# Kernel optimization log

Measured on AMD Instinct MI355X. Metric: run time of the kernel, lower is better.

## Reference

```python
import jax, jax.numpy as jnp
import numpy as np

M, K, N, G = 4096, 4096, 4096, 128


def setup_inputs() -> dict:
    key = jax.random.key(0)
    k1, k2, k3 = jax.random.split(key, 3)
    a = jax.random.normal(k1, (M, K), dtype=jnp.float16)
    # 4-bit unsigned quantized weights, values in [0, 16)
    w_q = jax.random.randint(k2, (K, N), 0, 16, dtype=jnp.int32)
    # group-wise scales: one per (k-group, n); small magnitude keeps fp16 output in range
    scale = jax.random.uniform(k3, (K // G, N), dtype=jnp.float16, minval=0.001, maxval=0.02)
    return {"a": a, "w_q": w_q, "scale": scale, "group_size": G}


def reference(a, w_q, scale, group_size):
    # Dequantize: w[k, n] = w_q[k, n] * scale[k // group_size, n]
    scale_full = jnp.repeat(scale, group_size, axis=0)  # [K, N]
    w = w_q.astype(a.dtype) * scale_full                # fp16 dequantized weight
    out = jnp.matmul(a, w, preferred_element_type=jnp.float32)
    return out.astype(jnp.float16)
```

## Files before the change

### kernel.cpp

```cpp
#include <hip/hip_runtime.h>
#include <hip/hip_fp16.h>

#define MDIM 4096
#define NDIM 4096
#define KDIM 4096

#define BM 128
#define BN 128
#define BK 64
#define NT 256

typedef _Float16 f16x8 __attribute__((ext_vector_type(8)));
typedef float f32x4 __attribute__((ext_vector_type(4)));
typedef unsigned int u32;
typedef unsigned short u16;

__device__ inline __half2 as_half2(u32 u) { return __builtin_bit_cast(__half2, u); }
__device__ inline u32 as_u32(__half2 h) { return __builtin_bit_cast(u32, h); }
__device__ inline u32 pkrtz(float a, float b) {
  return __builtin_bit_cast(u32, __builtin_amdgcn_cvt_pkrtz(a, b));
}

__device__ inline void load16_to_lds(const void* g, void* l) {
  __builtin_amdgcn_global_load_lds(
      (__attribute__((address_space(1))) const u32*)g,
      (__attribute__((address_space(3))) u32*)l,
      16, 0, 0);
}

__global__ __launch_bounds__(NT) void a_to_f16(const float* __restrict__ A,
                                               _Float16* __restrict__ A16) {
  const size_t base = ((size_t)blockIdx.x * NT + threadIdx.x) * 8;
  const float4 f0 = *(const float4*)(A + base);
  const float4 f1 = *(const float4*)(A + base + 4);
  u32 pk[4];
  pk[0] = pkrtz(f0.x, f0.y);
  pk[1] = pkrtz(f0.z, f0.w);
  pk[2] = pkrtz(f1.x, f1.y);
  pk[3] = pkrtz(f1.z, f1.w);
  *(uint4*)(A16 + base) = *(const uint4*)pk;
}

#define TSTR 68
__global__ __launch_bounds__(NT) void w_dequant_t(const int* __restrict__ Wq,
                                                  const float* __restrict__ Sc,
                                                  _Float16* __restrict__ Wt) {
  __shared__ __align__(16) u16 Ls[64 * TSTR];
  const int tid = threadIdx.x;
  const int n0 = (blockIdx.x & 63) * 64;
  const int k0 = (blockIdx.x >> 6) * 64;
  const int g = k0 >> 7;

#pragma unroll
  for (int r = 0; r < 4; ++r) {
    const int c = r * 256 + tid;
    const int krow = c >> 4;
    const int col4 = (c & 15) * 4;
    const int4 v = *(const int4*)(Wq + (size_t)(k0 + krow) * NDIM + n0 + col4);
    const float4 s = *(const float4*)(Sc + (size_t)g * NDIM + n0 + col4);
    __half2 s01 = __floats2half2_rn(s.x, s.y);
    __half2 s23 = __floats2half2_rn(s.z, s.w);
    const __half2 kneg = __half2half2(__float2half(-1024.0f));
    __half2 nb01 = __hmul2(s01, kneg), nb23 = __hmul2(s23, kneg);
    u32 u01 = (u32)v.x | ((u32)v.y << 16) | 0x64006400u;
    u32 u23 = (u32)v.z | ((u32)v.w << 16) | 0x64006400u;
    u32 pk[2];
    pk[0] = as_u32(__hfma2(as_half2(u01), s01, nb01));
    pk[1] = as_u32(__hfma2(as_half2(u23), s23, nb23));
    *(uint2*)&Ls[(size_t)krow * TSTR + col4] = *(const uint2*)pk;
  }
  __syncthreads();

#pragma unroll
  for (int r = 0; r < 2; ++r) {
    const int idx = r * 256 + tid;
    const int n = idx >> 3;
    const int kc = (idx & 7) * 8;
    u16 tmp[8];
#pragma unroll
    for (int j = 0; j < 8; ++j) tmp[j] = Ls[(size_t)(kc + j) * TSTR + n];
    *(uint4*)(Wt + (size_t)(n0 + n) * KDIM + k0 + kc) = *(const uint4*)tmp;
  }
}

__global__ __launch_bounds__(NT) void gemm_f16(const _Float16* __restrict__ A16,
                                               const _Float16* __restrict__ Wt,
                                               float* __restrict__ C) {
  __shared__ __align__(16) _Float16 As[BM * BK];
  __shared__ __align__(16) _Float16 Bs[BN * BK];

  const int tid = threadIdx.x;
  const int bx = blockIdx.x & 31;
  const int by = blockIdx.x >> 5;
  const int m_base = by * BM;
  const int n_base = bx * BN;

  const int wave = tid >> 6;
  const int lane = tid & 63;
  const int l15 = lane & 15;
  const int quad = lane >> 4;
  const int wm = (wave & 1) * 64;
  const int wn = (wave >> 1) * 64;

  f32x4 acc[4][4];
#pragma unroll
  for (int i = 0; i < 4; ++i)
#pragma unroll
    for (int j = 0; j < 4; ++j) acc[i][j] = (f32x4)0.0f;

  for (int kt = 0; kt < KDIM / BK; ++kt) {
    const int k0 = kt * BK;
    __syncthreads();

#pragma unroll
    for (int r = 0; r < 4; ++r) {
      const int c = r * 256 + tid;
      const int row = c >> 3;
      const int off = (c & 7) * 8;
      load16_to_lds(A16 + (size_t)(m_base + row) * KDIM + k0 + off,
                    (char*)As + (size_t)c * 16);
      load16_to_lds(Wt + (size_t)(n_base + row) * KDIM + k0 + off,
                    (char*)Bs + (size_t)c * 16);
    }
    __syncthreads();

#pragma unroll
    for (int ks = 0; ks < BK; ks += 32) {
      f16x8 af[4], bf[4];
#pragma unroll
      for (int i = 0; i < 4; ++i)
        af[i] = *(const f16x8*)&As[(size_t)(wm + i * 16 + l15) * BK + ks + quad * 8];
#pragma unroll
      for (int j = 0; j < 4; ++j)
        bf[j] = *(const f16x8*)&Bs[(size_t)(wn + j * 16 + l15) * BK + ks + quad * 8];
#pragma unroll
      for (int i = 0; i < 4; ++i)
#pragma unroll
        for (int j = 0; j < 4; ++j)
          acc[i][j] = __builtin_amdgcn_mfma_f32_16x16x32_f16(af[i], bf[j],
                                                             acc[i][j], 0, 0, 0);
    }
  }

#pragma unroll
  for (int i = 0; i < 4; ++i) {
#pragma unroll
    for (int j = 0; j < 4; ++j) {
      const int col = n_base + wn + j * 16 + l15;
#pragma unroll
      for (int r = 0; r < 4; ++r) {
        const int row = m_base + wm + i * 16 + quad * 4 + r;
        C[(size_t)row * NDIM + col] = __half2float(__float2half(acc[i][j][r]));
      }
    }
  }
}

#define STR 72
__global__ __launch_bounds__(NT) void qgemm_fused(
    const float* __restrict__ A, const int* __restrict__ Wq,
    const float* __restrict__ Sc, float* __restrict__ C) {
  __shared__ __align__(16) _Float16 As[BM * STR];
  __shared__ __align__(16) _Float16 Bs[BN * STR];
  const int tid = threadIdx.x;
  const int bx = blockIdx.x & 31, by = blockIdx.x >> 5;
  const int m_base = by * BM, n_base = bx * BN;
  const int wave = tid >> 6, lane = tid & 63;
  const int l15 = lane & 15, quad = lane >> 4;
  const int wm = (wave & 1) * 64, wn = (wave >> 1) * 64;
  const int bn_local = tid & 127, bk_half = (tid >> 7) * 8;
  const int gn = n_base + bn_local;
  f32x4 acc[4][4];
#pragma unroll
  for (int i = 0; i < 4; ++i)
#pragma unroll
    for (int j = 0; j < 4; ++j) acc[i][j] = (f32x4)0.0f;
  for (int kt = 0; kt < KDIM / BK; ++kt) {
    const int k0 = kt * BK;
    __syncthreads();
#pragma unroll
    for (int i = 0; i < 8; ++i) {
      const int c = i * 256 + tid;
      const int row = c >> 4, col4 = (c & 15) * 4;
      const float4 f = *(const float4*)(A + (size_t)(m_base + row) * KDIM + k0 + col4);
      u32 pk[2];
      pk[0] = pkrtz(f.x, f.y);
      pk[1] = pkrtz(f.z, f.w);
      *(uint2*)&As[(size_t)row * STR + col4] = *(const uint2*)pk;
    }
    {
      const __half hs = __float2half(Sc[(size_t)(k0 >> 7) * NDIM + gn]);
      const __half2 s2 = __half2half2(hs);
      const __half2 nb2 = __half2half2(__hmul(hs, __float2half(-1024.0f)));
#pragma unroll
      for (int it = 0; it < 4; ++it) {
        const int k = bk_half + it * 16;
        u32 v[8];
#pragma unroll
        for (int j = 0; j < 8; ++j)
          v[j] = (u32)Wq[(size_t)(k0 + k + j) * NDIM + gn];
        u32 pk[4];
#pragma unroll
        for (int p = 0; p < 4; ++p) {
          u32 u = v[2 * p] | (v[2 * p + 1] << 16) | 0x64006400u;
          pk[p] = as_u32(__hfma2(as_half2(u), s2, nb2));
        }
        *(uint4*)&Bs[(size_t)bn_local * STR + k] = *(const uint4*)pk;
      }
    }
    __syncthreads();
#pragma unroll
    for (int ks = 0; ks < BK; ks += 32) {
      f16x8 af[4], bf[4];
#pragma unroll
      for (int i = 0; i < 4; ++i)
        af[i] = *(const f16x8*)&As[(size_t)(wm + i * 16 + l15) * STR + ks + quad * 8];
#pragma unroll
      for (int j = 0; j < 4; ++j)
        bf[j] = *(const f16x8*)&Bs[(size_t)(wn + j * 16 + l15) * STR + ks + quad * 8];
#pragma unroll
      for (int i = 0; i < 4; ++i)
#pragma unroll
        for (int j = 0; j < 4; ++j)
          acc[i][j] = __builtin_amdgcn_mfma_f32_16x16x32_f16(af[i], bf[j],
                                                             acc[i][j], 0, 0, 0);
    }
  }
#pragma unroll
  for (int i = 0; i < 4; ++i)
#pragma unroll
    for (int j = 0; j < 4; ++j) {
      const int col = n_base + wn + j * 16 + l15;
#pragma unroll
      for (int r = 0; r < 4; ++r) {
        const int row = m_base + wm + i * 16 + quad * 4 + r;
        C[(size_t)row * NDIM + col] = __half2float(__float2half(acc[i][j][r]));
      }
    }
}

extern "C" void kernel_launch(void* const* d_in, const int* in_sizes, int n_in,
                              void* d_out, int out_size, void* d_ws, size_t ws_size,
                              hipStream_t stream) {
  const float* a = (const float*)d_in[0];
  const int* wq = (const int*)d_in[1];
  const float* sc = (const float*)d_in[2];
  float* out = (float*)d_out;

  const size_t a16_bytes = (size_t)MDIM * KDIM * 2;
  const size_t wt_bytes = (size_t)NDIM * KDIM * 2;

  if (ws_size >= a16_bytes + wt_bytes) {
    _Float16* a16 = (_Float16*)d_ws;
    _Float16* wt = (_Float16*)((char*)d_ws + a16_bytes);
    a_to_f16<<<(MDIM * (size_t)KDIM) / (NT * 8), NT, 0, stream>>>(a, a16);
    w_dequant_t<<<(KDIM / 64) * (NDIM / 64), NT, 0, stream>>>(wq, sc, wt);
    gemm_f16<<<(MDIM / BM) * (NDIM / BN), NT, 0, stream>>>(a16, wt, out);
  } else {
    qgemm_fused<<<(MDIM / BM) * (NDIM / BN), NT, 0, stream>>>(a, wq, sc, out);
  }
}
```

Baseline: 356.2 us.

## Merge prep kernels and XOR-swizzle LDS tiles to avoid bank conflicts

Combines the A fp32-to-fp16 conversion and the weight dequant/transpose into one launch, using block-index ranges to pick the work, which saves a kernel launch and its gap. In the GEMM it XOR-swizzles the 16-byte chunk column by row so that the MFMA fragment reads from LDS spread across banks instead of conflicting. Both the global-to-LDS load addressing and the fragment reads change, so the two must stay consistent.

```diff
diff --git a/kernel.cpp b/kernel.cpp
--- a/kernel.cpp
+++ b/kernel.cpp
@@ -28,25 +28,30 @@
       16, 0, 0);
 }
 
-__global__ __launch_bounds__(NT) void a_to_f16(const float* __restrict__ A,
-                                               _Float16* __restrict__ A16) {
-  const size_t base = ((size_t)blockIdx.x * NT + threadIdx.x) * 8;
-  const float4 f0 = *(const float4*)(A + base);
-  const float4 f1 = *(const float4*)(A + base + 4);
-  u32 pk[4];
-  pk[0] = pkrtz(f0.x, f0.y);
-  pk[1] = pkrtz(f0.z, f0.w);
-  pk[2] = pkrtz(f1.x, f1.y);
-  pk[3] = pkrtz(f1.z, f1.w);
-  *(uint4*)(A16 + base) = *(const uint4*)pk;
-}
-
 #define TSTR 68
-__global__ __launch_bounds__(NT) void w_dequant_t(const int* __restrict__ Wq,
-                                                  const float* __restrict__ Sc,
-                                                  _Float16* __restrict__ Wt) {
+#define WBLK 4096
+__global__ __launch_bounds__(NT) void prep(const float* __restrict__ A,
+                                           _Float16* __restrict__ A16,
+                                           const int* __restrict__ Wq,
+                                           const float* __restrict__ Sc,
+                                           _Float16* __restrict__ Wt) {
   __shared__ __align__(16) u16 Ls[64 * TSTR];
   const int tid = threadIdx.x;
+
+  if (blockIdx.x >= WBLK) {
+    const size_t b = blockIdx.x - WBLK;
+    const size_t base = (b * NT + tid) * 8;
+    const float4 f0 = *(const float4*)(A + base);
+    const float4 f1 = *(const float4*)(A + base + 4);
+    u32 pk[4];
+    pk[0] = pkrtz(f0.x, f0.y);
+    pk[1] = pkrtz(f0.z, f0.w);
+    pk[2] = pkrtz(f1.x, f1.y);
+    pk[3] = pkrtz(f1.z, f1.w);
+    *(uint4*)(A16 + base) = *(const uint4*)pk;
+    return;
+  }
+
   const int n0 = (blockIdx.x & 63) * 64;
   const int k0 = (blockIdx.x >> 6) * 64;
   const int g = k0 >> 7;
@@ -116,23 +121,30 @@
     for (int r = 0; r < 4; ++r) {
       const int c = r * 256 + tid;
       const int row = c >> 3;
-      const int off = (c & 7) * 8;
-      load16_to_lds(A16 + (size_t)(m_base + row) * KDIM + k0 + off,
+      const int gcol = (c & 7) ^ (row & 7);
+      load16_to_lds(A16 + (size_t)(m_base + row) * KDIM + k0 + gcol * 8,
                     (char*)As + (size_t)c * 16);
-      load16_to_lds(Wt + (size_t)(n_base + row) * KDIM + k0 + off,
+      load16_to_lds(Wt + (size_t)(n_base + row) * KDIM + k0 + gcol * 8,
                     (char*)Bs + (size_t)c * 16);
     }
     __syncthreads();
 
 #pragma unroll
     for (int ks = 0; ks < BK; ks += 32) {
+      const int ksc = ks >> 3;
       f16x8 af[4], bf[4];
 #pragma unroll
-      for (int i = 0; i < 4; ++i)
-        af[i] = *(const f16x8*)&As[(size_t)(wm + i * 16 + l15) * BK + ks + quad * 8];
-#pragma unroll
-      for (int j = 0; j < 4; ++j)
-        bf[j] = *(const f16x8*)&Bs[(size_t)(wn + j * 16 + l15) * BK + ks + quad * 8];
+      for (int i = 0; i < 4; ++i) {
+        const int row = wm + i * 16 + l15;
+        af[i] = *(const f16x8*)&As[((size_t)row * 8 +
+                                    ((ksc + quad) ^ (row & 7))) * 8];
+      }
+#pragma unroll
+      for (int j = 0; j < 4; ++j) {
+        const int row = wn + j * 16 + l15;
+        bf[j] = *(const f16x8*)&Bs[((size_t)row * 8 +
+                                    ((ksc + quad) ^ (row & 7))) * 8];
+      }
 #pragma unroll
       for (int i = 0; i < 4; ++i)
 #pragma unroll
@@ -253,8 +265,8 @@
   if (ws_size >= a16_bytes + wt_bytes) {
     _Float16* a16 = (_Float16*)d_ws;
     _Float16* wt = (_Float16*)((char*)d_ws + a16_bytes);
-    a_to_f16<<<(MDIM * (size_t)KDIM) / (NT * 8), NT, 0, stream>>>(a, a16);
-    w_dequant_t<<<(KDIM / 64) * (NDIM / 64), NT, 0, stream>>>(wq, sc, wt);
+    const int a_blocks = (MDIM * KDIM) / (NT * 8);
+    prep<<<WBLK + a_blocks, NT, 0, stream>>>(a, a16, wq, sc, wt);
     gemm_f16<<<(MDIM / BM) * (NDIM / BN), NT, 0, stream>>>(a16, wt, out);
   } else {
     qgemm_fused<<<(MDIM / BM) * (NDIM / BN), NT, 0, stream>>>(a, wq, sc, out);
```

Result: faster. 322.0 us (-9.6%).
